# Kernel tuning notes

Measured on AMD Instinct MI355X. Metric: run time of the kernel, lower is better.

## Reference

```python
import jax, jax.numpy as jnp
import numpy as np

N_NODES = 50000
N_EDGES = 800000
IN_DIM = 256
HID = 512
N_LAYERS = 3
OUT_DIM = 256
TOTAL_HID = HID * (N_LAYERS + 1)  # sum(hidden_dim) = 2048


def setup_inputs() -> dict:
    key = jax.random.key(0)
    ks = jax.random.split(key, 10)
    s = 0.02
    return {
        "x": jax.random.normal(ks[0], (N_NODES, IN_DIM), dtype=jnp.float32),
        "edge_index": jax.random.randint(ks[1], (2, N_EDGES), 0, N_NODES, dtype=jnp.int64),
        "in_W": jax.random.normal(ks[2], (IN_DIM, HID), dtype=jnp.float32) * s,
        "in_b": jnp.zeros((HID,), dtype=jnp.float32),
        "conv_W1": jax.random.normal(ks[3], (N_LAYERS, HID, HID), dtype=jnp.float32) * s,
        "conv_b1": jnp.zeros((N_LAYERS, HID), dtype=jnp.float32),
        "conv_W2": jax.random.normal(ks[4], (N_LAYERS, HID, HID), dtype=jnp.float32) * s,
        "conv_b2": jnp.zeros((N_LAYERS, HID), dtype=jnp.float32),
        "out_W": jax.random.normal(ks[5], (TOTAL_HID, OUT_DIM), dtype=jnp.float32) * s,
        "out_b": jnp.zeros((OUT_DIM,), dtype=jnp.float32),
    }


def reference(x, edge_index, in_W, in_b, conv_W1, conv_b1, conv_W2, conv_b2, out_W, out_b):
    src, dst = edge_index[0], edge_index[1]
    n = x.shape[0]
    # input projection
    h = x @ in_W + in_b
    hidden_states = [h]
    for i in range(N_LAYERS):
        # GINConv (eps=0): z = h + sum_{j in N(i)} h_j, then 2-layer MLP
        agg = jax.ops.segment_sum(h[src], dst, num_segments=n)  # [N, HID]
        z = h + agg
        z = jax.nn.relu(z @ conv_W1[i] + conv_b1[i])
        h = z @ conv_W2[i] + conv_b2[i]
        hidden_states.append(h)
    cat = jnp.concatenate(hidden_states, axis=1)  # [N, TOTAL_HID]
    return cat @ out_W + out_b
```

## Files before the change

kernel.cpp:

```cpp
#include <hip/hip_runtime.h>
#include <hip/hip_bf16.h>
#include <cstdint>
#include <cstddef>

typedef __bf16 bf16_t;
typedef __bf16 bf16x8 __attribute__((ext_vector_type(8)));
typedef float  f32x4  __attribute__((ext_vector_type(4)));
typedef int    int4a  __attribute__((ext_vector_type(4)));
typedef int    int4u  __attribute__((ext_vector_type(4), aligned(4)));

#define NN 50000
#define NNPAD 50176
#define NEDGE 800000
#define IND 256
#define HIDD 512
#define NLAYER 3
#define ODIM 256

#define AGG_CHUNK 224
#define AGG_NCH 224
#define SCAN_NB 49

__device__ __forceinline__ void gload16(const void* g, void* l) {
  __builtin_amdgcn_global_load_lds((const __attribute__((address_space(1))) void*)g,
                                   (__attribute__((address_space(3))) void*)l, 16, 0, 0);
}

__device__ __forceinline__ void xcd_bm_bn(int& bm, int& bn) {
  const int gN = gridDim.x;
  const int nwg = gN * gridDim.y;
  const int id = blockIdx.y * gN + blockIdx.x;
  const int q = nwg >> 3, r = nwg & 7;
  const int xcd = id & 7, loc = id >> 3;
  const int nid = (xcd < r ? xcd * (q + 1) : r * (q + 1) + (xcd - r) * q) + loc;
  bn = nid % gN;
  bm = nid / gN;
}

__global__ __launch_bounds__(256) void k_transpose_w(const float* __restrict__ W,
                                                     bf16_t* __restrict__ Wt,
                                                     int K, int N) {
  __shared__ float t[32][33];
  size_t zo = (size_t)blockIdx.z * K * N;
  const float* Wz = W + zo;
  bf16_t* Tz = Wt + zo;
  int bx = blockIdx.x * 32;
  int by = blockIdx.y * 32;
  int tx = threadIdx.x & 31, ty = threadIdx.x >> 5;
#pragma unroll
  for (int i = 0; i < 32; i += 8) {
    int k = by + ty + i, n = bx + tx;
    t[ty + i][tx] = (k < K && n < N) ? Wz[(size_t)k * N + n] : 0.f;
  }
  __syncthreads();
#pragma unroll
  for (int i = 0; i < 32; i += 8) {
    int n = bx + ty + i, k = by + tx;
    if (n < N && k < K) Tz[(size_t)n * K + k] = (bf16_t)t[tx][ty + i];
  }
}

__global__ void k_hist(const int* __restrict__ ei, int* __restrict__ cnt) {
  int e = blockIdx.x * 256 + threadIdx.x;
  if (e < NEDGE) atomicAdd(&cnt[ei[NEDGE + e]], 1);
}

__global__ __launch_bounds__(1024) void k_scan_local(const int* __restrict__ cnt,
                                                     int* __restrict__ off,
                                                     int* __restrict__ bsum) {
  __shared__ int s[1024];
  int b = blockIdx.x, tid = threadIdx.x;
  int idx = b * 1024 + tid;
  int v = (idx < NN) ? cnt[idx] : 0;
  s[tid] = v;
  __syncthreads();
  for (int d = 1; d < 1024; d <<= 1) {
    int t = (tid >= d) ? s[tid - d] : 0;
    __syncthreads();
    s[tid] += t;
    __syncthreads();
  }
  if (idx < NN) off[idx] = s[tid] - v;
  if (tid == 1023) bsum[b] = s[1023];
}

__global__ __launch_bounds__(64) void k_scan_bsum(const int* __restrict__ bsum,
                                                  int* __restrict__ boff,
                                                  int* __restrict__ off) {
  int lane = threadIdx.x & 63;
  int v = (lane < SCAN_NB) ? bsum[lane] : 0;
  int inc = v;
#pragma unroll
  for (int d = 1; d < 64; d <<= 1) {
    int t = __shfl_up(inc, d, 64);
    if (lane >= d) inc += t;
  }
  if (lane < SCAN_NB) boff[lane] = inc - v;
  if (lane == SCAN_NB - 1) off[NN] = inc;
}

__global__ __launch_bounds__(1024) void k_scan_add(const int* __restrict__ boff,
                                                   int* __restrict__ off) {
  int idx = blockIdx.x * 1024 + threadIdx.x;
  if (idx < NN) off[idx] += boff[blockIdx.x];
}

__global__ void k_scatter(const int* __restrict__ ei, const int* __restrict__ roff,
                          int* __restrict__ cnt, int* __restrict__ csr) {
  int e = blockIdx.x * 256 + threadIdx.x;
  if (e < NEDGE) {
    int d = ei[NEDGE + e];
    int p = atomicSub(&cnt[d], 1);
    csr[roff[d] + p - 1] = ei[e];
  }
}

__global__ __launch_bounds__(256) void k_aggregate_x(
    const bf16_t* __restrict__ h,
    const int* __restrict__ roff, const int* __restrict__ csr,
    bf16_t* __restrict__ z) {
  const int slice = blockIdx.x & 7;
  const int chunk = blockIdx.x >> 3;
  const int w = threadIdx.x >> 6;
  const int lane = threadIdx.x & 63;
  const int g = lane >> 3;
  const int gi = lane & 7;
  const int colb = slice * 64 + gi * 8;
  const bf16_t* hs = h + colb;
  const int nbase = chunk * AGG_CHUNK;
#pragma unroll 1
  for (int it = 0; it < AGG_CHUNK / 32; ++it) {
    int n = nbase + it * 32 + w * 8 + g;
    bool valid = n < NN;
    int o0 = valid ? roff[n] : 0;
    int o1 = valid ? roff[n + 1] : 0;
    bf16x8 hv;
    if (valid) hv = *(const bf16x8*)(hs + (size_t)n * HIDD);
    float acc[8];
#pragma unroll
    for (int j = 0; j < 8; j++) acc[j] = 0.f;
    int e = o0;
    for (; e + 4 <= o1; e += 4) {
      int4a s4 = *(const int4u*)(csr + e);
      bf16x8 v0 = *(const bf16x8*)(hs + (size_t)s4.x * HIDD);
      bf16x8 v1 = *(const bf16x8*)(hs + (size_t)s4.y * HIDD);
      bf16x8 v2 = *(const bf16x8*)(hs + (size_t)s4.z * HIDD);
      bf16x8 v3 = *(const bf16x8*)(hs + (size_t)s4.w * HIDD);
#pragma unroll
      for (int j = 0; j < 8; j++)
        acc[j] += ((float)v0[j] + (float)v1[j]) + ((float)v2[j] + (float)v3[j]);
    }
    for (; e < o1; ++e) {
      int s = csr[e];
      bf16x8 v = *(const bf16x8*)(hs + (size_t)s * HIDD);
#pragma unroll
      for (int j = 0; j < 8; j++) acc[j] += (float)v[j];
    }
    if (valid) {
      bf16x8 o;
#pragma unroll
      for (int j = 0; j < 8; j++) o[j] = (bf16_t)(acc[j] + (float)hv[j]);
      *(bf16x8*)(z + (size_t)n * HIDD + colb) = o;
    }
  }
}

__global__ __launch_bounds__(256) void k_gemm_in(
    const float* __restrict__ A, int lda, int M,
    const bf16_t* __restrict__ Bt, int K,
    const float* __restrict__ bias,
    bf16_t* __restrict__ Cb, int ldcb) {
  __shared__ char smem[32768] __attribute__((aligned(16)));
  char* ldsA = smem;
  char* ldsB = smem + 16384;

  const int tid = threadIdx.x;
  const int lane = tid & 63;
  const int w = tid >> 6;
  const int wr = w >> 1, wc = w & 1;
  const int lrow = lane & 15, lk = lane >> 4;
  int bm, bn;
  xcd_bm_bn(bm, bn);

  f32x4 acc[4][4];
#pragma unroll
  for (int m = 0; m < 4; m++)
#pragma unroll
    for (int n = 0; n < 4; n++) acc[m][n] = (f32x4){0.f, 0.f, 0.f, 0.f};

  const int srow = lane >> 3;
  const int sj = (lane & 7) ^ srow;
  const bf16_t* srcB = Bt + (size_t)(bn * 128 + srow) * K + sj * 8;

  const int ktiles = K >> 6;
  for (int kt = 0; kt < ktiles; ++kt) {
#pragma unroll
    for (int i = 0; i < 4; ++i) {
      int cb = i * 4 + w;
      gload16(srcB + (size_t)(cb * 8) * K + kt * 64, ldsB + cb * 1024);
    }
#pragma unroll
    for (int it = 0; it < 4; ++it) {
      int c = it * 256 + tid;
      int row = c >> 3, k8 = c & 7;
      int lo = (row * 128 + k8 * 16) ^ ((row & 7) << 4);
      int grow = bm * 128 + row;
      bf16x8 va;
#pragma unroll
      for (int j = 0; j < 8; j++) va[j] = (bf16_t)0.f;
      if (grow < M) {
        f32x4 u0 = *(const f32x4*)(A + (size_t)grow * lda + kt * 64 + k8 * 8);
        f32x4 u1 = *(const f32x4*)(A + (size_t)grow * lda + kt * 64 + k8 * 8 + 4);
#pragma unroll
        for (int j = 0; j < 4; j++) { va[j] = (bf16_t)u0[j]; va[4 + j] = (bf16_t)u1[j]; }
      }
      *(bf16x8*)(ldsA + lo) = va;
    }
    __syncthreads();
#pragma unroll
    for (int kk = 0; kk < 2; ++kk) {
      bf16x8 af[4], bfr[4];
#pragma unroll
      for (int m = 0; m < 4; m++) {
        int row = wr * 64 + m * 16 + lrow;
        af[m] = *(const bf16x8*)(ldsA + ((row * 128 + kk * 64 + lk * 16) ^ ((row & 7) << 4)));
      }
#pragma unroll
      for (int n = 0; n < 4; n++) {
        int col = wc * 64 + n * 16 + lrow;
        bfr[n] = *(const bf16x8*)(ldsB + ((col * 128 + kk * 64 + lk * 16) ^ ((col & 7) << 4)));
      }
#pragma unroll
      for (int m = 0; m < 4; m++)
#pragma unroll
        for (int n = 0; n < 4; n++)
          acc[m][n] = __builtin_amdgcn_mfma_f32_16x16x32_bf16(af[m], bfr[n], acc[m][n], 0, 0, 0);
    }
    __syncthreads();
  }
#pragma unroll
  for (int m = 0; m < 4; m++) {
    int rb = bm * 128 + wr * 64 + m * 16 + lk * 4;
#pragma unroll
    for (int n = 0; n < 4; n++) {
      int col = bn * 128 + wc * 64 + n * 16 + lrow;
      float bv = bias[col];
#pragma unroll
      for (int r = 0; r < 4; r++)
        Cb[(size_t)(rb + r) * ldcb + col] = (bf16_t)(acc[m][n][r] + bv);
    }
  }
}

template <int RELU>
__global__ __launch_bounds__(512) void k_gemm2(
    const bf16_t* __restrict__ A, int lda,
    const bf16_t* __restrict__ Bt, int K,
    const float* __restrict__ bias,
    bf16_t* __restrict__ Cb, int ldcb) {
  __shared__ char smem[65536] __attribute__((aligned(16)));

  const int tid = threadIdx.x;
  const int lane = tid & 63;
  const int w = tid >> 6;
  const int wr = w >> 1, wc = w & 1;
  const int lrow = lane & 15, lk = lane >> 4;
  int bm, bn;
  xcd_bm_bn(bm, bn);

  f32x4 acc[2][4];
#pragma unroll
  for (int m = 0; m < 2; m++)
#pragma unroll
    for (int n = 0; n < 4; n++) acc[m][n] = (f32x4){0.f, 0.f, 0.f, 0.f};

  const int srow = lane >> 3;
  const int sj = (lane & 7) ^ srow;
  const bf16_t* srcA = A + (size_t)(bm * 128 + srow) * lda + sj * 8;
  const bf16_t* srcB = Bt + (size_t)(bn * 128 + srow) * K + sj * 8;

  auto STAGE = [&](int kt, int buf) {
    char* lA = smem + buf * 32768;
    char* lB = lA + 16384;
#pragma unroll
    for (int i = 0; i < 2; ++i) {
      int c = i * 8 + w;
      gload16(srcA + (size_t)(c * 8) * lda + kt * 64, lA + c * 1024);
      gload16(srcB + (size_t)(c * 8) * K + kt * 64, lB + c * 1024);
    }
  };

  STAGE(0, 0);
  STAGE(1, 1);

  const int ktiles = K >> 6;
  int cur = 0;
  for (int kt = 0; kt < ktiles; ++kt) {
    if (kt == ktiles - 1) asm volatile("s_waitcnt vmcnt(0)" ::: "memory");
    else                  asm volatile("s_waitcnt vmcnt(4)" ::: "memory");
    __builtin_amdgcn_s_barrier();
    __builtin_amdgcn_sched_barrier(0);
    char* ldsA = smem + cur * 32768;
    char* ldsB = ldsA + 16384;
#pragma unroll
    for (int kk = 0; kk < 2; ++kk) {
      bf16x8 af[2], bfr[4];
#pragma unroll
      for (int m = 0; m < 2; m++) {
        int row = wr * 32 + m * 16 + lrow;
        af[m] = *(const bf16x8*)(ldsA + ((row * 128 + kk * 64 + lk * 16) ^ ((row & 7) << 4)));
      }
#pragma unroll
      for (int n = 0; n < 4; n++) {
        int col = wc * 64 + n * 16 + lrow;
        bfr[n] = *(const bf16x8*)(ldsB + ((col * 128 + kk * 64 + lk * 16) ^ ((col & 7) << 4)));
      }
#pragma unroll
      for (int m = 0; m < 2; m++)
#pragma unroll
        for (int n = 0; n < 4; n++)
          acc[m][n] = __builtin_amdgcn_mfma_f32_16x16x32_bf16(af[m], bfr[n], acc[m][n], 0, 0, 0);
    }
    asm volatile("s_waitcnt lgkmcnt(0)" ::: "memory");
    __builtin_amdgcn_s_barrier();
    __builtin_amdgcn_sched_barrier(0);
    if (kt + 2 < ktiles) STAGE(kt + 2, cur);
    cur ^= 1;
  }

#pragma unroll
  for (int m = 0; m < 2; m++) {
    int rb = bm * 128 + wr * 32 + m * 16 + lk * 4;
#pragma unroll
    for (int n = 0; n < 4; n++) {
      int col = bn * 128 + wc * 64 + n * 16 + lrow;
      float bv = bias[col];
#pragma unroll
      for (int r = 0; r < 4; r++) {
        float v = acc[m][n][r] + bv;
        if (RELU) v = fmaxf(v, 0.f);
        Cb[(size_t)(rb + r) * ldcb + col] = (bf16_t)v;
      }
    }
  }
}

template <int ACC>
__global__ __launch_bounds__(512) void k_gemm_out2(
    const bf16_t* __restrict__ A1, const bf16_t* __restrict__ A2, int lda,
    const bf16_t* __restrict__ B1t, const bf16_t* __restrict__ B2t, int K,
    const float* __restrict__ bias,
    float* __restrict__ Cf, int ldcf, int M) {
  __shared__ char smem[65536] __attribute__((aligned(16)));

  const int tid = threadIdx.x;
  const int lane = tid & 63;
  const int w = tid >> 6;
  const int wr = w >> 1, wc = w & 1;
  const int lrow = lane & 15, lk = lane >> 4;
  int bm, bn;
  xcd_bm_bn(bm, bn);

  f32x4 acc[2][4];
#pragma unroll
  for (int m = 0; m < 2; m++)
#pragma unroll
    for (int n = 0; n < 4; n++) acc[m][n] = (f32x4){0.f, 0.f, 0.f, 0.f};

  const int srow = lane >> 3;
  const int sj = (lane & 7) ^ srow;
  const size_t aoff = (size_t)(bm * 128 + srow) * lda + sj * 8;
  const size_t boff = (size_t)(bn * 128 + srow) * K + sj * 8;

  auto STAGE = [&](int kt, int buf) {
    const bf16_t* sA = (kt < 8 ? A1 : A2) + aoff + (kt & 7) * 64;
    const bf16_t* sB = (kt < 8 ? B1t : B2t) + boff + (kt & 7) * 64;
    char* lA = smem + buf * 32768;
    char* lB = lA + 16384;
#pragma unroll
    for (int i = 0; i < 2; ++i) {
      int c = i * 8 + w;
      gload16(sA + (size_t)(c * 8) * lda, lA + c * 1024);
      gload16(sB + (size_t)(c * 8) * K, lB + c * 1024);
    }
  };

  STAGE(0, 0);
  STAGE(1, 1);

  const int ktiles = 16;
  int cur = 0;
  for (int kt = 0; kt < ktiles; ++kt) {
    if (kt == ktiles - 1) asm volatile("s_waitcnt vmcnt(0)" ::: "memory");
    else                  asm volatile("s_waitcnt vmcnt(4)" ::: "memory");
    __builtin_amdgcn_s_barrier();
    __builtin_amdgcn_sched_barrier(0);
    char* ldsA = smem + cur * 32768;
    char* ldsB = ldsA + 16384;
#pragma unroll
    for (int kk = 0; kk < 2; ++kk) {
      bf16x8 af[2], bfr[4];
#pragma unroll
      for (int m = 0; m < 2; m++) {
        int row = wr * 32 + m * 16 + lrow;
        af[m] = *(const bf16x8*)(ldsA + ((row * 128 + kk * 64 + lk * 16) ^ ((row & 7) << 4)));
      }
#pragma unroll
      for (int n = 0; n < 4; n++) {
        int col = wc * 64 + n * 16 + lrow;
        bfr[n] = *(const bf16x8*)(ldsB + ((col * 128 + kk * 64 + lk * 16) ^ ((col & 7) << 4)));
      }
#pragma unroll
      for (int m = 0; m < 2; m++)
#pragma unroll
        for (int n = 0; n < 4; n++)
          acc[m][n] = __builtin_amdgcn_mfma_f32_16x16x32_bf16(af[m], bfr[n], acc[m][n], 0, 0, 0);
    }
    asm volatile("s_waitcnt lgkmcnt(0)" ::: "memory");
    __builtin_amdgcn_s_barrier();
    __builtin_amdgcn_sched_barrier(0);
    if (kt + 2 < ktiles) STAGE(kt + 2, cur);
    cur ^= 1;
  }

#pragma unroll
  for (int m = 0; m < 2; m++) {
    int rb = bm * 128 + wr * 32 + m * 16 + lk * 4;
#pragma unroll
    for (int n = 0; n < 4; n++) {
      int col = bn * 128 + wc * 64 + n * 16 + lrow;
      float bv = ACC ? 0.f : bias[col];
#pragma unroll
      for (int r = 0; r < 4; r++) {
        int row = rb + r;
        if (row < M) {
          float v = acc[m][n][r] + bv;
          if (ACC) Cf[(size_t)row * ldcf + col] += v;
          else     Cf[(size_t)row * ldcf + col] = v;
        }
      }
    }
  }
}

extern "C" void kernel_launch(void* const* d_in, const int* in_sizes, int n_in,
                              void* d_out, int out_size, void* d_ws, size_t ws_size,
                              hipStream_t stream) {
  const float* x    = (const float*)d_in[0];
  const int*   ei   = (const int*)d_in[1];
  const float* in_W = (const float*)d_in[2];
  const float* in_b = (const float*)d_in[3];
  const float* cW1  = (const float*)d_in[4];
  const float* cb1  = (const float*)d_in[5];
  const float* cW2  = (const float*)d_in[6];
  const float* cb2  = (const float*)d_in[7];
  const float* oW   = (const float*)d_in[8];
  const float* ob   = (const float*)d_in[9];
  float* out = (float*)d_out;

  char* ws = (char*)d_ws;
  size_t off = 0;
  auto alloc = [&](size_t bytes) -> char* {
    char* p = ws + off;
    off = (off + bytes + 255) & ~(size_t)255;
    return p;
  };
  bf16_t* bufA  = (bf16_t*)alloc((size_t)NNPAD * HIDD * 2);
  bf16_t* bufB  = (bf16_t*)alloc((size_t)NNPAD * HIDD * 2);
  bf16_t* bufC  = (bf16_t*)alloc((size_t)NNPAD * HIDD * 2);
  bf16_t* wt_in = (bf16_t*)alloc((size_t)IND * HIDD * 2);
  bf16_t* wt_c1 = (bf16_t*)alloc((size_t)NLAYER * HIDD * HIDD * 2);
  bf16_t* wt_c2 = (bf16_t*)alloc((size_t)NLAYER * HIDD * HIDD * 2);
  bf16_t* wt_ol = (bf16_t*)alloc((size_t)4 * ODIM * HIDD * 2);
  int* cnt  = (int*)alloc((size_t)NN * 4);
  int* roff = (int*)alloc((size_t)(NN + 1) * 4);
  int* csr  = (int*)alloc((size_t)NEDGE * 4);
  int* bsum = (int*)alloc((size_t)SCAN_NB * 4);
  int* boff = (int*)alloc((size_t)SCAN_NB * 4);

  hipMemsetAsync(cnt, 0, (size_t)NN * 4, stream);

  {
    dim3 g1((HIDD + 31) / 32, (IND + 31) / 32, 1);
    k_transpose_w<<<g1, 256, 0, stream>>>(in_W, wt_in, IND, HIDD);
    dim3 g2((HIDD + 31) / 32, (HIDD + 31) / 32, NLAYER);
    k_transpose_w<<<g2, 256, 0, stream>>>(cW1, wt_c1, HIDD, HIDD);
    k_transpose_w<<<g2, 256, 0, stream>>>(cW2, wt_c2, HIDD, HIDD);
    dim3 g3((ODIM + 31) / 32, (HIDD + 31) / 32, 4);
    k_transpose_w<<<g3, 256, 0, stream>>>(oW, wt_ol, HIDD, ODIM);
  }

  k_hist<<<(NEDGE + 255) / 256, 256, 0, stream>>>(ei, cnt);
  k_scan_local<<<SCAN_NB, 1024, 0, stream>>>(cnt, roff, bsum);
  k_scan_bsum<<<1, 64, 0, stream>>>(bsum, boff, roff);
  k_scan_add<<<SCAN_NB, 1024, 0, stream>>>(boff, roff);
  k_scatter<<<(NEDGE + 255) / 256, 256, 0, stream>>>(ei, roff, cnt, csr);

  dim3 gIn(HIDD / 128, NNPAD / 128);
  dim3 gH(HIDD / 128, NNPAD / 128);
  dim3 gO(ODIM / 128, NNPAD / 128);
  const int gAgg = 8 * AGG_NCH;

  k_gemm_in<<<gIn, 256, 0, stream>>>(x, IND, NN, wt_in, IND, in_b, bufA, HIDD);

  const size_t WW = (size_t)HIDD * HIDD;
  const size_t WO = (size_t)ODIM * HIDD;

  k_aggregate_x<<<gAgg, 256, 0, stream>>>(bufA, roff, csr, bufB);
  k_gemm2<1><<<gH, 512, 0, stream>>>(bufB, HIDD, wt_c1, HIDD, cb1, bufC, HIDD);
  k_gemm2<0><<<gH, 512, 0, stream>>>(bufC, HIDD, wt_c2, HIDD, cb2, bufB, HIDD);
  k_gemm_out2<0><<<gO, 512, 0, stream>>>(bufA, bufB, HIDD, wt_ol, wt_ol + WO, HIDD,
                                         ob, out, ODIM, NN);
  k_aggregate_x<<<gAgg, 256, 0, stream>>>(bufB, roff, csr, bufA);
  k_gemm2<1><<<gH, 512, 0, stream>>>(bufA, HIDD, wt_c1 + WW, HIDD, cb1 + HIDD, bufC, HIDD);
  k_gemm2<0><<<gH, 512, 0, stream>>>(bufC, HIDD, wt_c2 + WW, HIDD, cb2 + HIDD, bufA, HIDD);
  k_aggregate_x<<<gAgg, 256, 0, stream>>>(bufA, roff, csr, bufB);
  k_gemm2<1><<<gH, 512, 0, stream>>>(bufB, HIDD, wt_c1 + 2 * WW, HIDD, cb1 + 2 * HIDD, bufC, HIDD);
  k_gemm2<0><<<gH, 512, 0, stream>>>(bufC, HIDD, wt_c2 + 2 * WW, HIDD, cb2 + 2 * HIDD, bufB, HIDD);
  k_gemm_out2<1><<<gO, 512, 0, stream>>>(bufA, bufB, HIDD, wt_ol + 2 * WO, wt_ol + 3 * WO, HIDD,
                                         nullptr, out, ODIM, NN);
}
```

Before: 751.6 us.

## Replace fp32 input GEMM with bf16 conversion pass and shared gemm2 kernel

Removes the dedicated input-projection GEMM, which converted fp32 A tiles to bf16 inside its main loop. It now runs a separate elementwise fp32-to-bf16 conversion into a scratch buffer and reuses the 512-thread k_gemm2 kernel for the projection. The aggregation chunking also changes from 224 nodes per chunk to 64, which launches more, smaller aggregation blocks to improve load balance. The trade-off is an extra full pass over the input features, plus padded rows of the scratch buffer that are left unwritten and feed only padded GEMM rows.

```diff
diff --git a/kernel.cpp b/kernel.cpp
--- a/kernel.cpp
+++ b/kernel.cpp
@@ -17,8 +17,8 @@
 #define NLAYER 3
 #define ODIM 256
 
-#define AGG_CHUNK 224
-#define AGG_NCH 224
+#define AGG_CHUNK 64
+#define AGG_NCH 784
 #define SCAN_NB 49
 
 __device__ __forceinline__ void gload16(const void* g, void* l) {
@@ -57,6 +57,19 @@
   for (int i = 0; i < 32; i += 8) {
     int n = bx + ty + i, k = by + tx;
     if (n < N && k < K) Tz[(size_t)n * K + k] = (bf16_t)t[tx][ty + i];
+  }
+}
+
+__global__ __launch_bounds__(256) void k_convert(const float* __restrict__ x,
+                                                 bf16_t* __restrict__ y, int n8) {
+  int i = blockIdx.x * 256 + threadIdx.x;
+  if (i < n8) {
+    f32x4 u0 = *(const f32x4*)(x + (size_t)i * 8);
+    f32x4 u1 = *(const f32x4*)(x + (size_t)i * 8 + 4);
+    bf16x8 o;
+#pragma unroll
+    for (int j = 0; j < 4; j++) { o[j] = (bf16_t)u0[j]; o[4 + j] = (bf16_t)u1[j]; }
+    *(bf16x8*)(y + (size_t)i * 8) = o;
   }
 }
 
@@ -165,93 +178,6 @@
   }
 }
 
-__global__ __launch_bounds__(256) void k_gemm_in(
-    const float* __restrict__ A, int lda, int M,
-    const bf16_t* __restrict__ Bt, int K,
-    const float* __restrict__ bias,
-    bf16_t* __restrict__ Cb, int ldcb) {
-  __shared__ char smem[32768] __attribute__((aligned(16)));
-  char* ldsA = smem;
-  char* ldsB = smem + 16384;
-
-  const int tid = threadIdx.x;
-  const int lane = tid & 63;
-  const int w = tid >> 6;
-  const int wr = w >> 1, wc = w & 1;
-  const int lrow = lane & 15, lk = lane >> 4;
-  int bm, bn;
-  xcd_bm_bn(bm, bn);
-
-  f32x4 acc[4][4];
-#pragma unroll
-  for (int m = 0; m < 4; m++)
-#pragma unroll
-    for (int n = 0; n < 4; n++) acc[m][n] = (f32x4){0.f, 0.f, 0.f, 0.f};
-
-  const int srow = lane >> 3;
-  const int sj = (lane & 7) ^ srow;
-  const bf16_t* srcB = Bt + (size_t)(bn * 128 + srow) * K + sj * 8;
-
-  const int ktiles = K >> 6;
-  for (int kt = 0; kt < ktiles; ++kt) {
-#pragma unroll
-    for (int i = 0; i < 4; ++i) {
-      int cb = i * 4 + w;
-      gload16(srcB + (size_t)(cb * 8) * K + kt * 64, ldsB + cb * 1024);
-    }
-#pragma unroll
-    for (int it = 0; it < 4; ++it) {
-      int c = it * 256 + tid;
-      int row = c >> 3, k8 = c & 7;
-      int lo = (row * 128 + k8 * 16) ^ ((row & 7) << 4);
-      int grow = bm * 128 + row;
-      bf16x8 va;
-#pragma unroll
-      for (int j = 0; j < 8; j++) va[j] = (bf16_t)0.f;
-      if (grow < M) {
-        f32x4 u0 = *(const f32x4*)(A + (size_t)grow * lda + kt * 64 + k8 * 8);
-        f32x4 u1 = *(const f32x4*)(A + (size_t)grow * lda + kt * 64 + k8 * 8 + 4);
-#pragma unroll
-        for (int j = 0; j < 4; j++) { va[j] = (bf16_t)u0[j]; va[4 + j] = (bf16_t)u1[j]; }
-      }
-      *(bf16x8*)(ldsA + lo) = va;
-    }
-    __syncthreads();
-#pragma unroll
-    for (int kk = 0; kk < 2; ++kk) {
-      bf16x8 af[4], bfr[4];
-#pragma unroll
-      for (int m = 0; m < 4; m++) {
-        int row = wr * 64 + m * 16 + lrow;
-        af[m] = *(const bf16x8*)(ldsA + ((row * 128 + kk * 64 + lk * 16) ^ ((row & 7) << 4)));
-      }
-#pragma unroll
-      for (int n = 0; n < 4; n++) {
-        int col = wc * 64 + n * 16 + lrow;
-        bfr[n] = *(const bf16x8*)(ldsB + ((col * 128 + kk * 64 + lk * 16) ^ ((col & 7) << 4)));
-      }
-#pragma unroll
-      for (int m = 0; m < 4; m++)
-#pragma unroll
-        for (int n = 0; n < 4; n++)
-          acc[m][n] = __builtin_amdgcn_mfma_f32_16x16x32_bf16(af[m], bfr[n], acc[m][n], 0, 0, 0);
-    }
-    __syncthreads();
-  }
-#pragma unroll
-  for (int m = 0; m < 4; m++) {
-    int rb = bm * 128 + wr * 64 + m * 16 + lk * 4;
-#pragma unroll
-    for (int n = 0; n < 4; n++) {
-      int col = bn * 128 + wc * 64 + n * 16 + lrow;
-      float bv = bias[col];
-#pragma unroll
-      for (int r = 0; r < 4; r++)
-        Cb[(size_t)(rb + r) * ldcb + col] = (bf16_t)(acc[m][n][r] + bv);
-    }
-  }
-}
-
 template <int RELU>
 __global__ __launch_bounds__(512) void k_gemm2(
     const bf16_t* __restrict__ A, int lda,
@@ -496,12 +422,14 @@
   k_scan_add<<<SCAN_NB, 1024, 0, stream>>>(boff, roff);
   k_scatter<<<(NEDGE + 255) / 256, 256, 0, stream>>>(ei, roff, cnt, csr);
 
-  dim3 gIn(HIDD / 128, NNPAD / 128);
   dim3 gH(HIDD / 128, NNPAD / 128);
   dim3 gO(ODIM / 128, NNPAD / 128);
   const int gAgg = 8 * AGG_NCH;
 
-  k_gemm_in<<<gIn, 256, 0, stream>>>(x, IND, NN, wt_in, IND, in_b, bufA, HIDD);
+  bf16_t* xb = bufC;
+  k_convert<<<(NN * IND / 8 + 255) / 256, 256, 0, stream>>>(x, xb, NN * IND / 8);
+
+  k_gemm2<0><<<gH, 512, 0, stream>>>(xb, IND, wt_in, IND, in_b, bufA, HIDD);
 
   const size_t WW = (size_t)HIDD * HIDD;
   const size_t WO = (size_t)ODIM * HIDD;
```

New measurement: 739.0 us. About the same (-1.7%).
